# Optimization experiments

Hardware: AMD Instinct MI355X
Metric: run time of the kernel (lower is better)

Reference implementation:

```python
import jax, jax.numpy as jnp
import numpy as np

B = 65536
DIM = 8
HIS_LEN = 5
KIND_LEN = 10
HIS_ITEM_DIM = (1 + KIND_LEN) * DIM  # 88
ALL_DIM = DIM * (5 + KIND_LEN) + HIS_ITEM_DIM  # 208


def _linear_params(key, in_dim, out_dim):
    k1, k2 = jax.random.split(key)
    bound = 1.0 / np.sqrt(in_dim)
    w = jax.random.uniform(k1, (out_dim, in_dim), jnp.float32, -bound, bound)
    b = jax.random.uniform(k2, (out_dim,), jnp.float32, -bound, bound)
    return w, b


def setup_inputs() -> dict:
    key = jax.random.key(0)
    ks = jax.random.split(key, 20)
    inp = {
        'userid': jax.random.randint(ks[0], (B, 1), 0, 1000000),
        'itemid': jax.random.randint(ks[1], (B, 1), 0, 1000000),
        'user_age': jax.random.randint(ks[2], (B, 1), 0, 8),
        'gender': jax.random.randint(ks[3], (B, 1), 0, 3),
        'user_occupation': jax.random.randint(ks[4], (B, 1), 0, 25),
        'item_kind': jax.random.randint(ks[5], (B, KIND_LEN), 0, 20),
        'item_id_his': jax.random.randint(ks[6], (B, HIS_LEN), 0, 1000000),
        'item_kind_his': jax.random.randint(ks[7], (B, HIS_LEN, KIND_LEN), 0, 20),
        'user_emb': jax.random.normal(ks[8], (1000000, DIM), jnp.float32),
        'item_emb': jax.random.normal(ks[9], (1000000, DIM), jnp.float32),
        'age_emb': jax.random.normal(ks[10], (8, DIM), jnp.float32),
        'gender_emb': jax.random.normal(ks[11], (3, DIM), jnp.float32),
        'occ_emb': jax.random.normal(ks[12], (25, DIM), jnp.float32),
        'kind_emb': jax.random.normal(ks[13], (20, DIM), jnp.float32),
    }
    act_dims = [(HIS_ITEM_DIM * 3, 64), (64, 32), (32, 1)]
    for i, (di, do) in enumerate(act_dims, 1):
        w, b = _linear_params(jax.random.fold_in(key, 100 + i), di, do)
        inp[f'act_w{i}'], inp[f'act_b{i}'] = w, b
    mlp_dims = [(ALL_DIM, 128), (128, 64), (64, 32), (32, 1)]
    for i, (di, do) in enumerate(mlp_dims, 1):
        w, b = _linear_params(jax.random.fold_in(key, 200 + i), di, do)
        inp[f'mlp_w{i}'], inp[f'mlp_b{i}'] = w, b
    return inp


def _forward(userid, itemid, user_age, gender, user_occupation, item_kind,
             item_id_his, item_kind_his, user_emb, item_emb, age_emb,
             gender_emb, occ_emb, kind_emb,
             act_w1, act_b1, act_w2, act_b2, act_w3, act_b3,
             mlp_w1, mlp_b1, mlp_w2, mlp_b2, mlp_w3, mlp_b3, mlp_w4, mlp_b4):
    b = userid.shape[0]
    user_w = user_emb[userid]          # [b,1,8]
    item_w = item_emb[itemid]          # [b,1,8]
    age_w = age_emb[user_age]          # [b,1,8]
    gen_w = gender_emb[gender]         # [b,1,8]
    occ_w = occ_emb[user_occupation]   # [b,1,8]
    kind_w = kind_emb[item_kind]       # [b,10,8]
    kind_w = kind_w * (item_kind != 0)[..., None].astype(kind_w.dtype)

    # history: vectorized over his_len
    his_item_w = item_emb[item_id_his]           # [b,5,8]
    his_kind_w = kind_emb[item_kind_his]         # [b,5,10,8]
    his_kind_w = his_kind_w * (item_kind_his != 0)[..., None].astype(his_kind_w.dtype)
    his_feature = jnp.concatenate([his_item_w[:, :, None, :], his_kind_w], axis=2)
    his_feature = his_feature.reshape(b, HIS_LEN, HIS_ITEM_DIM)  # [b,5,88]

    item_feat_now = jnp.concatenate([item_w, kind_w], axis=1).reshape(b, 1, HIS_ITEM_DIM)
    item_feat_now = jnp.broadcast_to(item_feat_now, (b, HIS_LEN, HIS_ITEM_DIM))

    # ActUnit: i_in = [i1, i1-i2, i2]; score = MLP(i_in); act_weight = i1 * score
    i1, i2 = his_feature, item_feat_now
    i_in = jnp.concatenate([i1, i1 - i2, i2], axis=-1)  # [b,5,264]
    h = jax.nn.relu(jnp.einsum('bsd,od->bso', i_in, act_w1) + act_b1)
    h = jax.nn.relu(jnp.einsum('bsd,od->bso', h, act_w2) + act_b2)
    score = jnp.einsum('bsd,od->bso', h, act_w3) + act_b3  # [b,5,1]
    act_weight = i1 * score
    his_pool = jnp.sum(his_feature * act_weight, axis=1)  # [b,88]

    all_feat = jnp.concatenate([user_w, item_w, age_w, gen_w, occ_w, kind_w], axis=1).reshape(b, -1)
    all_feat = jnp.concatenate([all_feat, his_pool], axis=-1)  # [b,208]

    h = jax.nn.relu(all_feat @ mlp_w1.T + mlp_b1)
    h = jax.nn.relu(h @ mlp_w2.T + mlp_b2)
    h = jax.nn.relu(h @ mlp_w3.T + mlp_b3)
    logit = h @ mlp_w4.T + mlp_b4  # [b,1]
    return jax.nn.sigmoid(logit)


def reference(userid, itemid, user_age, gender, user_occupation, item_kind,
              item_id_his, item_kind_his, user_emb, item_emb, age_emb,
              gender_emb, occ_emb, kind_emb,
              act_w1, act_b1, act_w2, act_b2, act_w3, act_b3,
              mlp_w1, mlp_b1, mlp_w2, mlp_b2, mlp_w3, mlp_b3, mlp_w4, mlp_b4):
    return _forward(userid, itemid, user_age, gender, user_occupation, item_kind,
                    item_id_his, item_kind_his, user_emb, item_emb, age_emb,
                    gender_emb, occ_emb, kind_emb,
                    act_w1, act_b1, act_w2, act_b2, act_w3, act_b3,
                    mlp_w1, mlp_b1, mlp_w2, mlp_b2, mlp_w3, mlp_b3, mlp_w4, mlp_b4)
```

## Files before the change

### kernel.cpp

```cpp
#include <hip/hip_runtime.h>
#include <cstdint>
#include <math.h>

#define BATCH    65536
#define HIS_LEN  5
#define KIND_LEN 10
#define SB       128
#define NTH      512

typedef float    v2f __attribute__((ext_vector_type(2)));
typedef _Float16 v2h __attribute__((ext_vector_type(2)));
__device__ __forceinline__ v2f mk2(float a, float b){ v2f r; r.x=a; r.y=b; return r; }
#define C2H(u) __builtin_bit_cast(v2h,(unsigned)(u))

#if __has_builtin(__builtin_amdgcn_fdot2)
__device__ __forceinline__ float FD2(v2h a, v2h b, float c){
  return __builtin_amdgcn_fdot2(a, b, c, false);
}
#else
__device__ __forceinline__ float FD2(v2h a, v2h b, float c){
  return c + (float)a.x*(float)b.x + (float)a.y*(float)b.y;
}
#endif

__device__ __forceinline__ unsigned short f2h(float f){
  return __builtin_bit_cast(unsigned short, (_Float16)f);
}
__device__ __forceinline__ float h2f(unsigned short s){
  return (float)__builtin_bit_cast(_Float16, s);
}
__device__ __forceinline__ unsigned pack2h(float a, float b){
  return (unsigned)f2h(a) | ((unsigned)f2h(b) << 16);
}
__device__ __forceinline__ v2h pkh(float a, float b){
  return __builtin_bit_cast(v2h, __builtin_amdgcn_cvt_pkrtz(a, b));
}

#define OFF_WC1H 0
#define OFF_AB1  6144
#define OFF_W2T  6208
#define OFF_AB2  8256
#define OFF_W3   8288
#define OFF_AB3  8320
#define OFF_M1H  8324
#define OFF_MB1  22660
#define OFF_M2T  22788
#define OFF_MB2  30980
#define OFF_M3T  31044
#define OFF_MB3  33092
#define OFF_M4   33124
#define OFF_MB4  33156
#define PREP_N   33157
#define M1H4  2081
#define M2T4  5697
#define M3T4  7761

#define PFF   6144
#define W2TF4 1552
#define MBB   8450
#define TPF   8466
#define LDSF  12562

typedef const float* fp;

__device__ __forceinline__ float m1s_val(fp m1, int o, int q, int t){
  if(t >= 52) return 0.f;
  int src;
  if(t<8){ int E = (q==0)?0:(8+8*q); src = E + t; }
  else if(t<30){ int d=t-8; int idx = 8*(d>>1)+2*q+(d&1);
                 src = (idx<8) ? (8+idx) : (32+idx); }
  else { int d=t-30; int idx = 8*(d>>1)+2*q+(d&1); src = 120+idx; }
  return m1[o*208 + src];
}
__device__ __forceinline__ float w1c_val(fp aw1, int o, int q, int h, int d){
  if(d >= 22) return 0.f;
  int idx = 8*(d>>1) + 2*q + (d&1);
  return h ? (aw1[o*264+176+idx] - aw1[o*264+88+idx])
           : (aw1[o*264+idx]     + aw1[o*264+88+idx]);
}

__global__ void din_prep(fp aw1, fp ab1, fp aw2, fp ab2, fp aw3, fp ab3,
                         fp m1,  fp mb1, fp m2,  fp mb2, fp m3,  fp mb3,
                         fp m4,  fp mb4, float* __restrict__ ws){
  int j = blockIdx.x*blockDim.x + threadIdx.x;
  unsigned* wsu = (unsigned*)ws;
  if(j < 6144){
    int h = j/3072, r = j%3072;
    int slot = r/12, dw = r - slot*12;
    int o = slot>>2, q = slot&3;
    wsu[OFF_WC1H + j] = pack2h(w1c_val(aw1,o,q,h,2*dw), w1c_val(aw1,o,q,h,2*dw+1));
    return;
  } j -= 6144;
  if(j < 64){ ws[OFF_AB1 + j] = ab1[j]; return; } j -= 64;
  if(j < 2048){ int o=j/32, p=j%32; ws[OFF_W2T + j] = aw2[p*64 + o]; return; } j -= 2048;
  if(j < 32){ ws[OFF_AB2 + j] = ab2[j]; return; } j -= 32;
  if(j < 32){ ws[OFF_W3  + j] = aw3[j]; return; } j -= 32;
  if(j < 1){ ws[OFF_AB3] = ab3[0]; return; } j -= 1;
  if(j < 3){ ws[OFF_AB3+1+j] = 0.f; return; } j -= 3;
  if(j < 14336){
    int slot = j/28, dw = j - slot*28;
    int o = slot>>2, q = slot&3;
    wsu[OFF_M1H + j] = pack2h(m1s_val(m1,o,q,2*dw), m1s_val(m1,o,q,2*dw+1));
    return;
  } j -= 14336;
  if(j < 128){ ws[OFF_MB1 + j] = mb1[j]; return; } j -= 128;
  if(j < 8192){ int o=j/64, p=j%64; ws[OFF_M2T + j] = m2[p*128 + o]; return; } j -= 8192;
  if(j < 64){ ws[OFF_MB2 + j] = mb2[j]; return; } j -= 64;
  if(j < 2048){ int o=j/32, p=j%32; ws[OFF_M3T + j] = m3[p*64 + o]; return; } j -= 2048;
  if(j < 32){ ws[OFF_MB3 + j] = mb3[j]; return; } j -= 32;
  if(j < 32){ ws[OFF_M4  + j] = m4[j];  return; } j -= 32;
  if(j < 1){ ws[OFF_MB4] = mb4[0]; return; }
}

template<int CTL>
__device__ __forceinline__ float qp(float v){
  return __uint_as_float((unsigned)__builtin_amdgcn_update_dpp(
      0, (int)__float_as_uint(v), CTL, 0xF, 0xF, true));
}
__device__ __forceinline__ float bsum4(float v){
  v += qp<0xB1>(v);
  v += qp<0x4E>(v);
  return v;
}

__device__ __forceinline__ void ldst16(void* l, const void* g){
  __builtin_amdgcn_global_load_lds(
      (const __attribute__((address_space(1))) unsigned int*)(uintptr_t)g,
      (__attribute__((address_space(3))) unsigned int*)(uintptr_t)l, 16, 0, 0);
}
__device__ __forceinline__ void ldst4(void* l, const void* g){
  __builtin_amdgcn_global_load_lds(
      (const __attribute__((address_space(1))) unsigned int*)(uintptr_t)g,
      (__attribute__((address_space(3))) unsigned int*)(uintptr_t)l, 4, 0, 0);
}

__device__ __forceinline__ void gather_h(const float2* __restrict__ itemp,
                                         const float2* __restrict__ kindp,
                                         int item_idx, const int* __restrict__ kidx,
                                         int q, v2h* f){
  float2 v = itemp[item_idx*4 + q];
  f[0] = pkh(v.x, v.y);
  #pragma unroll
  for(int r=0;r<KIND_LEN;r++){
    int ki = kidx[r];
    float2 w = kindp[ki*4 + q];
    float mx = ki ? w.x : 0.f, my = ki ? w.y : 0.f;
    f[1+r] = pkh(mx, my);
  }
}

#define PKF(acc, a, b, vv) do{ (acc) = __builtin_elementwise_fma(mk2((a),(b)), (vv), (acc)); }while(0)

template<int NS>
__device__ __forceinline__ void hist_pass(int b, int s0, int q, int wid,
    const float2* __restrict__ item_emb, const float2* __restrict__ kind_emb,
    const int* __restrict__ his_id, const int* __restrict__ his_kind,
    const float* ls, const float4* ls4, const unsigned short* tp, v2f* poolv){
  v2h i1h[NS][11];
  #pragma unroll
  for(int t=0;t<NS;t++)
    gather_h(item_emb, kind_emb, his_id[b*HIS_LEN + s0 + t],
             his_kind + (b*HIS_LEN + s0 + t)*KIND_LEN, q, i1h[t]);
  v2f h2v[NS][4];
  #pragma unroll
  for(int t=0;t<NS;t++)
    #pragma unroll
    for(int j=0;j<4;j++) h2v[t][j] = mk2(0.f,0.f);

  #pragma unroll 1
  for(int oo=0;oo<64;oo++){
    const uint4* wr = (const uint4*)(ls4 + (oo*4+q)*3);
    uint4 r0 = wr[0], r1 = wr[1], r2 = wr[2];
    unsigned dwv[12] = {r0.x,r0.y,r0.z,r0.w, r1.x,r1.y,r1.z,r1.w, r2.x,r2.y,r2.z,r2.w};
    float t2b = h2f(tp[oo*SB + wid]);
    float aA[NS], aB[NS];
    #pragma unroll
    for(int t=0;t<NS;t++){ aA[t]=0.f; aB[t]=0.f; }
    #pragma unroll
    for(int u=0;u<11;u++){
      #pragma unroll
      for(int t=0;t<NS;t++){
        if(u&1) aB[t] = FD2(C2H(dwv[u]), i1h[t][u], aB[t]);
        else    aA[t] = FD2(C2H(dwv[u]), i1h[t][u], aA[t]);
      }
    }
    float4 wa = ls4[W2TF4 + oo*8 + 2*q];
    float4 wb = ls4[W2TF4 + 1 + oo*8 + 2*q];
    #pragma unroll
    for(int t=0;t<NS;t++){
      float h = bsum4(aA[t]+aB[t]) + t2b;
      h = fmaxf(h, 0.f);
      v2f hh = mk2(h, h);
      PKF(h2v[t][0], wa.x, wa.y, hh);
      PKF(h2v[t][1], wa.z, wa.w, hh);
      PKF(h2v[t][2], wb.x, wb.y, hh);
      PKF(h2v[t][3], wb.z, wb.w, hh);
    }
  }
  #pragma unroll
  for(int t=0;t<NS;t++){
    float scp = 0.f;
    #pragma unroll
    for(int jj=0;jj<4;jj++){
      float hx = fmaxf(h2v[t][jj].x + ls[PFF+2112+8*q+2*jj],   0.f);
      float hy = fmaxf(h2v[t][jj].y + ls[PFF+2112+8*q+2*jj+1], 0.f);
      scp += ls[PFF+2144+8*q+2*jj]*hx + ls[PFF+2144+8*q+2*jj+1]*hy;
    }
    float sc = bsum4(scp) + ls[PFF+2176];
    #pragma unroll
    for(int j=0;j<11;j++){
      float sx = (float)i1h[t][j].x, sy = (float)i1h[t][j].y;
      poolv[j] = __builtin_elementwise_fma(mk2(sx*sc, sy*sc), mk2(sx, sy), poolv[j]);
    }
  }
}

__device__ __forceinline__ void mlp_stage(int c, int tid, float* ls, float4* ls4,
                                          const float* ws, const float4* ws4){
  int base = 768 + (c&1)*384;
  if(tid < 352){
    const float4* src = (tid < 224) ? (ws4 + M1H4 + c*224 + tid)
                                    : (ws4 + M2T4 + c*128 + (tid-224));
    ldst16(ls4 + base + tid, src);
  }
  if(tid < 8) ldst4(ls + MBB + (c&1)*8 + tid, ws + OFF_MB1 + c*8 + tid);
}

__global__ void __launch_bounds__(NTH, 4)
din_main(const int* __restrict__ userid, const int* __restrict__ itemid,
         const int* __restrict__ age,    const int* __restrict__ gen,
         const int* __restrict__ occ,    const int* __restrict__ item_kind,
         const int* __restrict__ his_id, const int* __restrict__ his_kind,
         const float2* __restrict__ user_emb, const float2* __restrict__ item_emb,
         const float2* __restrict__ age_emb,  const float2* __restrict__ gen_emb,
         const float2* __restrict__ occ_emb,  const float2* __restrict__ kind_emb,
         const float* __restrict__ ws, float* __restrict__ out){
  const int tid  = threadIdx.x;
  const int q    = tid & 3;
  const int sl   = (tid & 63) >> 2;
  const int wv   = __builtin_amdgcn_readfirstlane(tid >> 6);
  const int wid  = wv*16 + sl;
  const int b    = blockIdx.x*SB + wid;

  __shared__ __align__(16) float ls[LDSF];
  float4* ls4 = (float4*)ls;
  const float* wsc = ws;
  const float4* ws4 = (const float4*)ws;
  unsigned short* tp = (unsigned short*)(ls + TPF);

  #pragma unroll
  for(int k=0;k<4;k++){ int j = k*NTH + tid; ldst4(ls + PFF + j, wsc + OFF_AB1 + j); }
  if(tid < 129) ldst4(ls + PFF + 2048 + tid, wsc + OFF_AB1 + 2048 + tid);
  if(tid < 64)  ldst4(ls + PFF + 2177 + tid, wsc + OFF_MB2 + tid);
  if(tid < 65)  ldst4(ls + PFF + 2241 + tid, wsc + OFF_MB3 + tid);
  #pragma unroll
  for(int k=0;k<3;k++){ int j = k*NTH + tid; ldst16(ls4 + j, ws4 + j); }

  v2h i2h[11];
  gather_h(item_emb, kind_emb, itemid[b], item_kind + b*KIND_LEN, q, i2h);

  __syncthreads();

  #pragma unroll 2
  for(int oo=0;oo<64;oo++){
    const uint4* wr = (const uint4*)(ls4 + 768 + (oo*4+q)*3);
    uint4 r0 = wr[0], r1 = wr[1], r2 = wr[2];
    unsigned dwv[12] = {r0.x,r0.y,r0.z,r0.w, r1.x,r1.y,r1.z,r1.w, r2.x,r2.y,r2.z,r2.w};
    float aA = 0.f, aB = 0.f;
    #pragma unroll
    for(int u=0;u<11;u++){
      if(u&1) aB = FD2(C2H(dwv[u]), i2h[u], aB);
      else    aA = FD2(C2H(dwv[u]), i2h[u], aA);
    }
    float s = bsum4(aA+aB);
    if(q==0) tp[oo*SB + wid] = f2h(s + ls[PFF + oo]);
  }

  __syncthreads();

  mlp_stage(0, tid, ls, ls4, wsc, ws4);
  mlp_stage(1, tid, ls, ls4, wsc, ws4);

  v2f poolv[11];
  #pragma unroll
  for(int d=0;d<11;d++) poolv[d]=mk2(0.f,0.f);
  hist_pass<2>(b, 0, q, wid, item_emb, kind_emb, his_id, his_kind, ls, ls4, tp, poolv);
  hist_pass<2>(b, 2, q, wid, item_emb, kind_emb, his_id, his_kind, ls, ls4, tp, poolv);
  hist_pass<1>(b, 4, q, wid, item_emb, kind_emb, his_id, his_kind, ls, ls4, tp, poolv);

  v2h poolh[11];
  #pragma unroll
  for(int j=0;j<11;j++) poolh[j] = pkh(poolv[j].x, poolv[j].y);
  v2h fe[26];
  {
    const float2* ep = (q==0)? user_emb : (q==1)? age_emb : (q==2)? gen_emb : occ_emb;
    int ei = (q==0)? userid[b] : (q==1)? age[b] : (q==2)? gen[b] : occ[b];
    #pragma unroll
    for(int k=0;k<4;k++){ float2 v = ep[ei*4+k]; fe[k] = pkh(v.x, v.y); }
  }
  #pragma unroll
  for(int j=0;j<11;j++) fe[4+j]  = i2h[j];
  #pragma unroll
  for(int j=0;j<11;j++) fe[15+j] = poolh[j];
  v2f h2m[8];
  #pragma unroll
  for(int j=0;j<8;j++) h2m[j] = mk2(ls[PFF+2177+16*q+2*j], ls[PFF+2177+16*q+2*j+1]);

  __syncthreads();

  #pragma unroll 1
  for(int c=0;c<16;c++){
    int base = 768 + (c&1)*384;
    #pragma unroll 1
    for(int i=0;i<8;i++){
      const uint4* wr = (const uint4*)(ls4 + base + (i*4+q)*7);
      unsigned dwv[28];
      #pragma unroll
      for(int k=0;k<7;k++){
        uint4 t = wr[k];
        dwv[4*k]=t.x; dwv[4*k+1]=t.y; dwv[4*k+2]=t.z; dwv[4*k+3]=t.w;
      }
      float aA = 0.f, aB = 0.f;
      #pragma unroll
      for(int u=0;u<26;u++){
        if(u&1) aB = FD2(C2H(dwv[u]), fe[u], aB);
        else    aA = FD2(C2H(dwv[u]), fe[u], aA);
      }
      float h = fmaxf(bsum4(aA+aB) + ls[MBB + (c&1)*8 + i], 0.f);
      v2f hh = mk2(h, h);
      const float4* w2 = ls4 + base + 224 + i*16 + 4*q;
      #pragma unroll
      for(int k=0;k<4;k++){
        float4 w = w2[k];
        PKF(h2m[2*k],   w.x, w.y, hh);
        PKF(h2m[2*k+1], w.z, w.w, hh);
      }
    }
    __syncthreads();
    if(c < 14){
      mlp_stage(c+2, tid, ls, ls4, wsc, ws4);
    } else if(c == 14){
      int j = tid;
      ldst16(ls4 + (j>>7)*130 + (j&127), ws4 + M3T4 + j);
    }
  }

  float hv[16];
  #pragma unroll
  for(int j=0;j<16;j++) hv[j] = fmaxf((j&1) ? h2m[j>>1].y : h2m[j>>1].x, 0.f);

  float x = ls[PFF+2305];
  #pragma unroll
  for(int g=0;g<4;g++){
    float a[8];
    #pragma unroll
    for(int j=0;j<8;j++) a[j]=0.f;
    #pragma unroll
    for(int i=0;i<16;i++){
      float4 wA = ls4[q*130 + i*8 + 2*g];
      float4 wB = ls4[q*130 + i*8 + 2*g + 1];
      a[0]+=wA.x*hv[i]; a[1]+=wA.y*hv[i]; a[2]+=wA.z*hv[i]; a[3]+=wA.w*hv[i];
      a[4]+=wB.x*hv[i]; a[5]+=wB.y*hv[i]; a[6]+=wB.z*hv[i]; a[7]+=wB.w*hv[i];
    }
    #pragma unroll
    for(int j=0;j<8;j++) a[j] = bsum4(a[j]);
    #pragma unroll
    for(int j=0;j<8;j++)
      x += ls[PFF+2273+8*g+j] * fmaxf(a[j] + ls[PFF+2241+8*g+j], 0.f);
  }

  if(q==0) out[b] = 1.0f/(1.0f + __expf(-x));
}

extern "C" void kernel_launch(void* const* d_in, const int* in_sizes, int n_in,
                              void* d_out, int out_size, void* d_ws, size_t ws_size,
                              hipStream_t stream){
  const int* userid    = (const int*)d_in[0];
  const int* itemid    = (const int*)d_in[1];
  const int* age       = (const int*)d_in[2];
  const int* gen       = (const int*)d_in[3];
  const int* occ       = (const int*)d_in[4];
  const int* item_kind = (const int*)d_in[5];
  const int* his_id    = (const int*)d_in[6];
  const int* his_kind  = (const int*)d_in[7];
  const float2* user_emb = (const float2*)d_in[8];
  const float2* item_emb = (const float2*)d_in[9];
  const float2* age_emb  = (const float2*)d_in[10];
  const float2* gen_emb  = (const float2*)d_in[11];
  const float2* occ_emb  = (const float2*)d_in[12];
  const float2* kind_emb = (const float2*)d_in[13];
  float* ws = (float*)d_ws;

  din_prep<<<(PREP_N+255)/256, 256, 0, stream>>>(
      (fp)d_in[14], (fp)d_in[15], (fp)d_in[16], (fp)d_in[17], (fp)d_in[18], (fp)d_in[19],
      (fp)d_in[20], (fp)d_in[21], (fp)d_in[22], (fp)d_in[23], (fp)d_in[24], (fp)d_in[25],
      (fp)d_in[26], (fp)d_in[27], ws);

  din_main<<<BATCH/SB, NTH, 0, stream>>>(
      userid, itemid, age, gen, occ, item_kind, his_id, his_kind,
      user_emb, item_emb, age_emb, gen_emb, occ_emb, kind_emb,
      ws, (float*)d_out);
}
```

Measured before the change: 290.5 us.

## Pack second-layer weights to fp16 and use fdot2 for all small GEMVs

Converts the second attention layer, second MLP layer and third MLP layer weights to packed fp16 pairs. Hidden activations are paired into half2 so those layers run on fdot2 instead of packed fp32 FMA. The workspace and LDS layouts are reorganised to match, and the attention first-layer loops now process two outputs per iteration. This cuts the LDS footprint, the weight-staging traffic and the ALU work per element, at the cost of lower intermediate precision.

```diff
diff --git a/kernel.cpp b/kernel.cpp
--- a/kernel.cpp
+++ b/kernel.cpp
@@ -26,9 +26,6 @@
 __device__ __forceinline__ unsigned short f2h(float f){
   return __builtin_bit_cast(unsigned short, (_Float16)f);
 }
-__device__ __forceinline__ float h2f(unsigned short s){
-  return (float)__builtin_bit_cast(_Float16, s);
-}
 __device__ __forceinline__ unsigned pack2h(float a, float b){
   return (unsigned)f2h(a) | ((unsigned)f2h(b) << 16);
 }
@@ -38,28 +35,30 @@
 
 #define OFF_WC1H 0
 #define OFF_AB1  6144
-#define OFF_W2T  6208
-#define OFF_AB2  8256
-#define OFF_W3   8288
-#define OFF_AB3  8320
-#define OFF_M1H  8324
-#define OFF_MB1  22660
-#define OFF_M2T  22788
-#define OFF_MB2  30980
-#define OFF_M3T  31044
-#define OFF_MB3  33092
-#define OFF_M4   33124
-#define OFF_MB4  33156
-#define PREP_N   33157
-#define M1H4  2081
-#define M2T4  5697
-#define M3T4  7761
+#define OFF_W2H  7208
+#undef  OFF_W2H
+#define OFF_W2H  6208
+#define OFF_AB2  7232
+#define OFF_W3   7264
+#define OFF_AB3  7296
+#define OFF_MB2  7297
+#define OFF_MB3  7361
+#define OFF_M4   7393
+#define OFF_MB4  7425
+#define OFF_M3H  7428
+#define OFF_M1H  8452
+#define OFF_MB1  22788
+#define OFF_M2H  22916
+#define PREP_N   27012
+#define M1H4  2113
+#define M2H4  5729
+#define M3H4  1857
 
 #define PFF   6144
-#define W2TF4 1552
-#define MBB   8450
-#define TPF   8466
-#define LDSF  12562
+#define W2HF4 1552
+#define MBB   7426
+#define TPF   7442
+#define LDSF  11538
 
 typedef const float* fp;
 
@@ -92,11 +91,25 @@
     return;
   } j -= 6144;
   if(j < 64){ ws[OFF_AB1 + j] = ab1[j]; return; } j -= 64;
-  if(j < 2048){ int o=j/32, p=j%32; ws[OFF_W2T + j] = aw2[p*64 + o]; return; } j -= 2048;
+  if(j < 1024){
+    int pp = j>>5, q = (j>>3)&3, dw = j&7;
+    int o = 8*q + dw;
+    wsu[OFF_W2H + j] = pack2h(aw2[o*64 + 2*pp], aw2[o*64 + 2*pp+1]);
+    return;
+  } j -= 1024;
   if(j < 32){ ws[OFF_AB2 + j] = ab2[j]; return; } j -= 32;
   if(j < 32){ ws[OFF_W3  + j] = aw3[j]; return; } j -= 32;
   if(j < 1){ ws[OFF_AB3] = ab3[0]; return; } j -= 1;
-  if(j < 3){ ws[OFF_AB3+1+j] = 0.f; return; } j -= 3;
+  if(j < 64){ ws[OFF_MB2 + j] = mb2[j]; return; } j -= 64;
+  if(j < 32){ ws[OFF_MB3 + j] = mb3[j]; return; } j -= 32;
+  if(j < 32){ ws[OFF_M4  + j] = m4[j];  return; } j -= 32;
+  if(j < 1){ ws[OFF_MB4] = mb4[0]; return; } j -= 1;
+  if(j < 2){ ws[7426 + j] = 0.f; return; } j -= 2;
+  if(j < 1024){
+    int qq = j>>8, rr = j&255, ip = rr>>5, dw = rr&31;
+    wsu[OFF_M3H + j] = pack2h(m3[dw*64 + 16*qq + 2*ip], m3[dw*64 + 16*qq + 2*ip+1]);
+    return;
+  } j -= 1024;
   if(j < 14336){
     int slot = j/28, dw = j - slot*28;
     int o = slot>>2, q = slot&3;
@@ -104,12 +117,12 @@
     return;
   } j -= 14336;
   if(j < 128){ ws[OFF_MB1 + j] = mb1[j]; return; } j -= 128;
-  if(j < 8192){ int o=j/64, p=j%64; ws[OFF_M2T + j] = m2[p*128 + o]; return; } j -= 8192;
-  if(j < 64){ ws[OFF_MB2 + j] = mb2[j]; return; } j -= 64;
-  if(j < 2048){ int o=j/32, p=j%32; ws[OFF_M3T + j] = m3[p*64 + o]; return; } j -= 2048;
-  if(j < 32){ ws[OFF_MB3 + j] = mb3[j]; return; } j -= 32;
-  if(j < 32){ ws[OFF_M4  + j] = m4[j];  return; } j -= 32;
-  if(j < 1){ ws[OFF_MB4] = mb4[0]; return; }
+  if(j < 4096){
+    int gp = j>>6, q = (j>>4)&3, dw = j&15;
+    int o = 16*q + dw;
+    wsu[OFF_M2H + j] = pack2h(m2[o*128 + 2*gp], m2[o*128 + 2*gp+1]);
+    return;
+  }
 }
 
 template<int CTL>
@@ -149,64 +162,61 @@
   }
 }
 
-#define PKF(acc, a, b, vv) do{ (acc) = __builtin_elementwise_fma(mk2((a),(b)), (vv), (acc)); }while(0)
-
 template<int NS>
 __device__ __forceinline__ void hist_pass(int b, int s0, int q, int wid,
     const float2* __restrict__ item_emb, const float2* __restrict__ kind_emb,
     const int* __restrict__ his_id, const int* __restrict__ his_kind,
-    const float* ls, const float4* ls4, const unsigned short* tp, v2f* poolv){
+    const float* ls, const float4* ls4, const unsigned* tpu, v2f* poolv){
   v2h i1h[NS][11];
   #pragma unroll
   for(int t=0;t<NS;t++)
     gather_h(item_emb, kind_emb, his_id[b*HIS_LEN + s0 + t],
              his_kind + (b*HIS_LEN + s0 + t)*KIND_LEN, q, i1h[t]);
-  v2f h2v[NS][4];
+  float h2s[NS][8];
   #pragma unroll
   for(int t=0;t<NS;t++)
     #pragma unroll
-    for(int j=0;j<4;j++) h2v[t][j] = mk2(0.f,0.f);
+    for(int k=0;k<8;k++) h2s[t][k] = 0.f;
 
   #pragma unroll 1
-  for(int oo=0;oo<64;oo++){
-    const uint4* wr = (const uint4*)(ls4 + (oo*4+q)*3);
-    uint4 r0 = wr[0], r1 = wr[1], r2 = wr[2];
-    unsigned dwv[12] = {r0.x,r0.y,r0.z,r0.w, r1.x,r1.y,r1.z,r1.w, r2.x,r2.y,r2.z,r2.w};
-    float t2b = h2f(tp[oo*SB + wid]);
-    float aA[NS], aB[NS];
-    #pragma unroll
-    for(int t=0;t<NS;t++){ aA[t]=0.f; aB[t]=0.f; }
-    #pragma unroll
-    for(int u=0;u<11;u++){
+  for(int p=0;p<32;p++){
+    const uint4* wr0 = (const uint4*)(ls4 + ((2*p  )*4+q)*3);
+    const uint4* wr1 = (const uint4*)(ls4 + ((2*p+1)*4+q)*3);
+    uint4 r0=wr0[0], r1=wr0[1], r2=wr0[2];
+    uint4 s0v=wr1[0], s1v=wr1[1], s2v=wr1[2];
+    unsigned w0[12] = {r0.x,r0.y,r0.z,r0.w, r1.x,r1.y,r1.z,r1.w, r2.x,r2.y,r2.z,r2.w};
+    unsigned w1[12] = {s0v.x,s0v.y,s0v.z,s0v.w, s1v.x,s1v.y,s1v.z,s1v.w, s2v.x,s2v.y,s2v.z,s2v.w};
+    v2h t2 = C2H(tpu[p*SB + wid]);
+    v2h hpv[NS];
+    #pragma unroll
+    for(int t=0;t<NS;t++){
+      float aA=0.f, aB=0.f, cA=0.f, cB=0.f;
       #pragma unroll
-      for(int t=0;t<NS;t++){
-        if(u&1) aB[t] = FD2(C2H(dwv[u]), i1h[t][u], aB[t]);
-        else    aA[t] = FD2(C2H(dwv[u]), i1h[t][u], aA[t]);
+      for(int u=0;u<11;u++){
+        if(u&1){ aB = FD2(C2H(w0[u]), i1h[t][u], aB); cB = FD2(C2H(w1[u]), i1h[t][u], cB); }
+        else   { aA = FD2(C2H(w0[u]), i1h[t][u], aA); cA = FD2(C2H(w1[u]), i1h[t][u], cA); }
       }
-    }
-    float4 wa = ls4[W2TF4 + oo*8 + 2*q];
-    float4 wb = ls4[W2TF4 + 1 + oo*8 + 2*q];
-    #pragma unroll
-    for(int t=0;t<NS;t++){
-      float h = bsum4(aA[t]+aB[t]) + t2b;
-      h = fmaxf(h, 0.f);
-      v2f hh = mk2(h, h);
-      PKF(h2v[t][0], wa.x, wa.y, hh);
-      PKF(h2v[t][1], wa.z, wa.w, hh);
-      PKF(h2v[t][2], wb.x, wb.y, hh);
-      PKF(h2v[t][3], wb.z, wb.w, hh);
-    }
+      float h0 = fmaxf(bsum4(aA+aB) + (float)t2.x, 0.f);
+      float h1 = fmaxf(bsum4(cA+cB) + (float)t2.y, 0.f);
+      hpv[t] = pkh(h0, h1);
+    }
+    uint4 wa = *(const uint4*)(ls4 + W2HF4 + (p*4+q)*2);
+    uint4 wb = *(const uint4*)(ls4 + W2HF4 + (p*4+q)*2 + 1);
+    unsigned w2d[8] = {wa.x,wa.y,wa.z,wa.w, wb.x,wb.y,wb.z,wb.w};
+    #pragma unroll
+    for(int t=0;t<NS;t++)
+      #pragma unroll
+      for(int k=0;k<8;k++) h2s[t][k] = FD2(C2H(w2d[k]), hpv[t], h2s[t][k]);
   }
   #pragma unroll
   for(int t=0;t<NS;t++){
     float scp = 0.f;
     #pragma unroll
-    for(int jj=0;jj<4;jj++){
-      float hx = fmaxf(h2v[t][jj].x + ls[PFF+2112+8*q+2*jj],   0.f);
-      float hy = fmaxf(h2v[t][jj].y + ls[PFF+2112+8*q+2*jj+1], 0.f);
-      scp += ls[PFF+2144+8*q+2*jj]*hx + ls[PFF+2144+8*q+2*jj+1]*hy;
-    }
-    float sc = bsum4(scp) + ls[PFF+2176];
+    for(int j=0;j<8;j++){
+      float hx = fmaxf(h2s[t][j] + ls[PFF+1088+8*q+j], 0.f);
+      scp += ls[PFF+1120+8*q+j]*hx;
+    }
+    float sc = bsum4(scp) + ls[PFF+1152];
     #pragma unroll
     for(int j=0;j<11;j++){
       float sx = (float)i1h[t][j].x, sy = (float)i1h[t][j].y;
@@ -217,10 +227,10 @@
 
 __device__ __forceinline__ void mlp_stage(int c, int tid, float* ls, float4* ls4,
                                           const float* ws, const float4* ws4){
-  int base = 768 + (c&1)*384;
-  if(tid < 352){
+  int base = 768 + (c&1)*288;
+  if(tid < 288){
     const float4* src = (tid < 224) ? (ws4 + M1H4 + c*224 + tid)
-                                    : (ws4 + M2T4 + c*128 + (tid-224));
+                                    : (ws4 + M2H4 + c*64 + (tid-224));
     ldst16(ls4 + base + tid, src);
   }
   if(tid < 8) ldst4(ls + MBB + (c&1)*8 + tid, ws + OFF_MB1 + c*8 + tid);
@@ -246,13 +256,12 @@
   float4* ls4 = (float4*)ls;
   const float* wsc = ws;
   const float4* ws4 = (const float4*)ws;
-  unsigned short* tp = (unsigned short*)(ls + TPF);
-
-  #pragma unroll
-  for(int k=0;k<4;k++){ int j = k*NTH + tid; ldst4(ls + PFF + j, wsc + OFF_AB1 + j); }
-  if(tid < 129) ldst4(ls + PFF + 2048 + tid, wsc + OFF_AB1 + 2048 + tid);
-  if(tid < 64)  ldst4(ls + PFF + 2177 + tid, wsc + OFF_MB2 + tid);
-  if(tid < 65)  ldst4(ls + PFF + 2241 + tid, wsc + OFF_MB3 + tid);
+  unsigned* tpu = (unsigned*)(ls + TPF);
+
+  #pragma unroll
+  for(int k=0;k<2;k++){ int j = k*NTH + tid; ldst4(ls + PFF + j, wsc + OFF_AB1 + j); }
+  { int j = 2*NTH + tid;
+    if(j < 1282) ldst4(ls + PFF + j, wsc + OFF_AB1 + j); }
   #pragma unroll
   for(int k=0;k<3;k++){ int j = k*NTH + tid; ldst16(ls4 + j, ws4 + j); }
 
@@ -261,19 +270,25 @@
 
   __syncthreads();
 
-  #pragma unroll 2
-  for(int oo=0;oo<64;oo++){
-    const uint4* wr = (const uint4*)(ls4 + 768 + (oo*4+q)*3);
-    uint4 r0 = wr[0], r1 = wr[1], r2 = wr[2];
-    unsigned dwv[12] = {r0.x,r0.y,r0.z,r0.w, r1.x,r1.y,r1.z,r1.w, r2.x,r2.y,r2.z,r2.w};
-    float aA = 0.f, aB = 0.f;
+  #pragma unroll 1
+  for(int p=0;p<32;p++){
+    const uint4* wr0 = (const uint4*)(ls4 + 768 + ((2*p  )*4+q)*3);
+    const uint4* wr1 = (const uint4*)(ls4 + 768 + ((2*p+1)*4+q)*3);
+    uint4 r0=wr0[0], r1=wr0[1], r2=wr0[2];
+    uint4 s0v=wr1[0], s1v=wr1[1], s2v=wr1[2];
+    unsigned w0[12] = {r0.x,r0.y,r0.z,r0.w, r1.x,r1.y,r1.z,r1.w, r2.x,r2.y,r2.z,r2.w};
+    unsigned w1[12] = {s0v.x,s0v.y,s0v.z,s0v.w, s1v.x,s1v.y,s1v.z,s1v.w, s2v.x,s2v.y,s2v.z,s2v.w};
+    float aA=0.f, aB=0.f, cA=0.f, cB=0.f;
     #pragma unroll
     for(int u=0;u<11;u++){
-      if(u&1) aB = FD2(C2H(dwv[u]), i2h[u], aB);
-      else    aA = FD2(C2H(dwv[u]), i2h[u], aA);
-    }
-    float s = bsum4(aA+aB);
-    if(q==0) tp[oo*SB + wid] = f2h(s + ls[PFF + oo]);
+      if(u&1){ aB = FD2(C2H(w0[u]), i2h[u], aB); cB = FD2(C2H(w1[u]), i2h[u], cB); }
+      else   { aA = FD2(C2H(w0[u]), i2h[u], aA); cA = FD2(C2H(w1[u]), i2h[u], cA); }
+    }
+    float sA = bsum4(aA+aB), sB = bsum4(cA+cB);
+    if(q==0){
+      float2 bb = ((const float2*)(ls+PFF))[p];
+      tpu[p*SB + wid] = __builtin_bit_cast(unsigned, pkh(sA+bb.x, sB+bb.y));
+    }
   }
 
   __syncthreads();
@@ -284,13 +299,10 @@
   v2f poolv[11];
   #pragma unroll
   for(int d=0;d<11;d++) poolv[d]=mk2(0.f,0.f);
-  hist_pass<2>(b, 0, q, wid, item_emb, kind_emb, his_id, his_kind, ls, ls4, tp, poolv);
-  hist_pass<2>(b, 2, q, wid, item_emb, kind_emb, his_id, his_kind, ls, ls4, tp, poolv);
-  hist_pass<1>(b, 4, q, wid, item_emb, kind_emb, his_id, his_kind, ls, ls4, tp, poolv);
-
-  v2h poolh[11];
-  #pragma unroll
-  for(int j=0;j<11;j++) poolh[j] = pkh(poolv[j].x, poolv[j].y);
+  hist_pass<2>(b, 0, q, wid, item_emb, kind_emb, his_id, his_kind, ls, ls4, tpu, poolv);
+  hist_pass<2>(b, 2, q, wid, item_emb, kind_emb, his_id, his_kind, ls, ls4, tpu, poolv);
+  hist_pass<1>(b, 4, q, wid, item_emb, kind_emb, his_id, his_kind, ls, ls4, tpu, poolv);
+
   v2h fe[26];
   {
     const float2* ep = (q==0)? user_emb : (q==1)? age_emb : (q==2)? gen_emb : occ_emb;
@@ -301,72 +313,78 @@
   #pragma unroll
   for(int j=0;j<11;j++) fe[4+j]  = i2h[j];
   #pragma unroll
-  for(int j=0;j<11;j++) fe[15+j] = poolh[j];
-  v2f h2m[8];
-  #pragma unroll
-  for(int j=0;j<8;j++) h2m[j] = mk2(ls[PFF+2177+16*q+2*j], ls[PFF+2177+16*q+2*j+1]);
+  for(int j=0;j<11;j++) fe[15+j] = pkh(poolv[j].x, poolv[j].y);
+  float h2s2[16];
+  #pragma unroll
+  for(int k=0;k<16;k++) h2s2[k] = ls[PFF+1153+16*q+k];
 
   __syncthreads();
 
   #pragma unroll 1
   for(int c=0;c<16;c++){
-    int base = 768 + (c&1)*384;
+    int base = 768 + (c&1)*288;
     #pragma unroll 1
-    for(int i=0;i<8;i++){
-      const uint4* wr = (const uint4*)(ls4 + base + (i*4+q)*7);
-      unsigned dwv[28];
+    for(int ii=0;ii<4;ii++){
+      float hh[2];
       #pragma unroll
-      for(int k=0;k<7;k++){
-        uint4 t = wr[k];
-        dwv[4*k]=t.x; dwv[4*k+1]=t.y; dwv[4*k+2]=t.z; dwv[4*k+3]=t.w;
+      for(int e=0;e<2;e++){
+        int i = 2*ii + e;
+        const uint4* wr = (const uint4*)(ls4 + base + (i*4+q)*7);
+        unsigned dwv[28];
+        #pragma unroll
+        for(int k=0;k<7;k++){
+          uint4 t = wr[k];
+          dwv[4*k]=t.x; dwv[4*k+1]=t.y; dwv[4*k+2]=t.z; dwv[4*k+3]=t.w;
+        }
+        float aA = 0.f, aB = 0.f;
+        #pragma unroll
+        for(int u=0;u<26;u++){
+          if(u&1) aB = FD2(C2H(dwv[u]), fe[u], aB);
+          else    aA = FD2(C2H(dwv[u]), fe[u], aA);
+        }
+        hh[e] = fmaxf(bsum4(aA+aB) + ls[MBB + (c&1)*8 + i], 0.f);
       }
-      float aA = 0.f, aB = 0.f;
+      v2h hp = pkh(hh[0], hh[1]);
+      const uint4* w2p = (const uint4*)(ls4 + base + 224 + (ii*4+q)*4);
+      uint4 a0=w2p[0], a1=w2p[1], a2=w2p[2], a3=w2p[3];
+      unsigned d2[16] = {a0.x,a0.y,a0.z,a0.w, a1.x,a1.y,a1.z,a1.w,
+                         a2.x,a2.y,a2.z,a2.w, a3.x,a3.y,a3.z,a3.w};
       #pragma unroll
-      for(int u=0;u<26;u++){
-        if(u&1) aB = FD2(C2H(dwv[u]), fe[u], aB);
-        else    aA = FD2(C2H(dwv[u]), fe[u], aA);
-      }
-      float h = fmaxf(bsum4(aA+aB) + ls[MBB + (c&1)*8 + i], 0.f);
-      v2f hh = mk2(h, h);
-      const float4* w2 = ls4 + base + 224 + i*16 + 4*q;
-      #pragma unroll
-      for(int k=0;k<4;k++){
-        float4 w = w2[k];
-        PKF(h2m[2*k],   w.x, w.y, hh);
-        PKF(h2m[2*k+1], w.z, w.w, hh);
-      }
+      for(int k=0;k<16;k++) h2s2[k] = FD2(C2H(d2[k]), hp, h2s2[k]);
     }
     __syncthreads();
     if(c < 14){
       mlp_stage(c+2, tid, ls, ls4, wsc, ws4);
     } else if(c == 14){
-      int j = tid;
-      ldst16(ls4 + (j>>7)*130 + (j&127), ws4 + M3T4 + j);
-    }
-  }
-
-  float hv[16];
-  #pragma unroll
-  for(int j=0;j<16;j++) hv[j] = fmaxf((j&1) ? h2m[j>>1].y : h2m[j>>1].x, 0.f);
-
-  float x = ls[PFF+2305];
+      if(tid < 256) ldst16(ls4 + (tid>>6)*66 + (tid&63), ws4 + M3H4 + tid);
+    }
+  }
+
+  v2h hp3[8];
+  #pragma unroll
+  for(int ip=0;ip<8;ip++)
+    hp3[ip] = pkh(fmaxf(h2s2[2*ip],0.f), fmaxf(h2s2[2*ip+1],0.f));
+
+  float x = ls[PFF+1281];
   #pragma unroll
   for(int g=0;g<4;g++){
     float a[8];
     #pragma unroll
     for(int j=0;j<8;j++) a[j]=0.f;
     #pragma unroll
-    for(int i=0;i<16;i++){
-      float4 wA = ls4[q*130 + i*8 + 2*g];
-      float4 wB = ls4[q*130 + i*8 + 2*g + 1];
-      a[0]+=wA.x*hv[i]; a[1]+=wA.y*hv[i]; a[2]+=wA.z*hv[i]; a[3]+=wA.w*hv[i];
-      a[4]+=wB.x*hv[i]; a[5]+=wB.y*hv[i]; a[6]+=wB.z*hv[i]; a[7]+=wB.w*hv[i];
+    for(int ip=0;ip<8;ip++){
+      const uint4* w3p = (const uint4*)(ls4 + q*66 + ip*8 + 2*g);
+      uint4 b0=w3p[0], b1=w3p[1];
+      a[0]=FD2(C2H(b0.x),hp3[ip],a[0]); a[1]=FD2(C2H(b0.y),hp3[ip],a[1]);
+      a[2]=FD2(C2H(b0.z),hp3[ip],a[2]); a[3]=FD2(C2H(b0.w),hp3[ip],a[3]);
+      a[4]=FD2(C2H(b1.x),hp3[ip],a[4]); a[5]=FD2(C2H(b1.y),hp3[ip],a[5]);
+      a[6]=FD2(C2H(b1.z),hp3[ip],a[6]); a[7]=FD2(C2H(b1.w),hp3[ip],a[7]);
     }
     #pragma unroll
     for(int j=0;j<8;j++) a[j] = bsum4(a[j]);
     #pragma unroll
     for(int j=0;j<8;j++)
-      x += ls[PFF+2273+8*g+j] * fmaxf(a[j] + ls[PFF+2241+8*g+j], 0.f);
+      x += ls[PFF+1249+8*g+j] * fmaxf(a[j] + ls[PFF+1217+8*g+j], 0.f);
   }
 
   if(q==0) out[b] = 1.0f/(1.0f + __expf(-x));
```

Measured after the change: 285.4 us. About the same (-1.8%).
